# Kernel tuning notes

Measured on AMD Instinct MI355X. Metric: run time of the kernel, lower is better.

## Reference

```python
import jax, jax.numpy as jnp
import numpy as np
import math

D = 1024
H = 16
EPS = 1e-5

def _layernorm(x, gamma, beta):
    mu = jnp.mean(x, axis=-1, keepdims=True)
    var = jnp.var(x, axis=-1, keepdims=True)
    return (x - mu) * jax.lax.rsqrt(var + EPS) * gamma + beta

def setup_inputs() -> dict:
    key = jax.random.key(0)
    ks = jax.random.split(key, 6)
    B, T = 2, 2048
    x = jax.random.normal(ks[0], (B, T, D), dtype=jnp.float32)
    s = 1.0 / math.sqrt(D)
    Wq = jax.random.normal(ks[1], (D, D), dtype=jnp.float32) * s
    Wk = jax.random.normal(ks[2], (D, D), dtype=jnp.float32) * s
    Wv = jax.random.normal(ks[3], (D, D), dtype=jnp.float32) * s
    gamma = jnp.ones((D,), dtype=jnp.float32)
    beta = jnp.zeros((D,), dtype=jnp.float32)
    return {"x": x, "Wq": Wq, "Wk": Wk, "Wv": Wv, "gamma": gamma, "beta": beta}

def reference(x, Wq, Wk, Wv, gamma, beta):
    B, T, Dm = x.shape
    hd = Dm // H
    xn = _layernorm(x, gamma, beta)
    # torch Linear (no bias): y = x @ W.T
    q = (xn @ Wq.T).reshape(B, T, H, hd)
    k = (xn @ Wk.T).reshape(B, T, H, hd)
    v = (xn @ Wv.T).reshape(B, T, H, hd)
    scale = 1.0 / math.sqrt(hd)
    att = jnp.einsum('bnhd,bmhd->bnmh', q, k) * scale  # B,T,T,H
    w = jax.nn.softmax(att, axis=2)  # softmax over key dim m
    y = jnp.einsum('bnmh,bmhd->bnhd', w, v).reshape(B, T, Dm)
    return x + y
```

## Files before the change

kernel.cpp:

```cpp
#include <hip/hip_runtime.h>
#include <hip/hip_bf16.h>
#include <stdint.h>

#define D_MODEL 1024
#define T_SEQ   2048
#define NB      2
#define NH      16
#define HD      64
#define MTOK    4096

typedef __bf16  bf16x8 __attribute__((ext_vector_type(8)));
typedef float   f32x4  __attribute__((ext_vector_type(4)));
typedef float   f32x16 __attribute__((ext_vector_type(16)));

#define GPTR(p) ((const __attribute__((address_space(1))) void*)(p))
#define LPTR(p) ((__attribute__((address_space(3))) void*)(p))

static __device__ __forceinline__ ushort f2bf(float f) {
    union { float f; uint32_t u; } c{f};
    uint32_t u = c.u;
    return (ushort)((u + 0x7fff + ((u >> 16) & 1)) >> 16);
}

static __device__ __forceinline__ unsigned cvt_pk_bf16(float lo, float hi) {
    unsigned r;
    asm("v_cvt_pk_bf16_f32 %0, %1, %2" : "=v"(r) : "v"(lo), "v"(hi));
    return r;
}

#if defined(__has_builtin)
#if __has_builtin(__builtin_amdgcn_exp2f)
#define FEXP2(x) __builtin_amdgcn_exp2f(x)
#endif
#endif
#ifndef FEXP2
static __device__ __forceinline__ float fexp2_asm(float x) {
    float r;
    asm("v_exp_f32 %0, %1" : "=v"(r) : "v"(x));
    return r;
}
#define FEXP2(x) fexp2_asm(x)
#endif

__global__ __launch_bounds__(256) void ln_kernel(const float* __restrict__ x,
                                                 const float* __restrict__ gamma,
                                                 const float* __restrict__ beta,
                                                 ushort* __restrict__ xn) {
    int row = blockIdx.x;
    int tid = threadIdx.x;
    const float4* xr = (const float4*)(x + (size_t)row * D_MODEL);
    float4 v = xr[tid];
    float s  = v.x + v.y + v.z + v.w;
    float ss = v.x * v.x + v.y * v.y + v.z * v.z + v.w * v.w;
    #pragma unroll
    for (int m = 1; m < 64; m <<= 1) {
        s  += __shfl_xor(s, m);
        ss += __shfl_xor(ss, m);
    }
    __shared__ float red[8];
    int w = tid >> 6, lane = tid & 63;
    if (lane == 0) { red[w] = s; red[4 + w] = ss; }
    __syncthreads();
    s  = red[0] + red[1] + red[2] + red[3];
    ss = red[4] + red[5] + red[6] + red[7];
    float mu   = s * (1.0f / D_MODEL);
    float var  = ss * (1.0f / D_MODEL) - mu * mu;
    float rstd = rsqrtf(var + 1e-5f);
    float4 g = ((const float4*)gamma)[tid];
    float4 b = ((const float4*)beta)[tid];
    ushort4 o;
    o.x = f2bf((v.x - mu) * rstd * g.x + b.x);
    o.y = f2bf((v.y - mu) * rstd * g.y + b.y);
    o.z = f2bf((v.z - mu) * rstd * g.z + b.z);
    o.w = f2bf((v.w - mu) * rstd * g.w + b.w);
    ((ushort4*)(xn + (size_t)row * D_MODEL))[tid] = o;
}

__global__ __launch_bounds__(256) void cvt3_kernel(const float* __restrict__ a0,
                                                   const float* __restrict__ a1,
                                                   const float* __restrict__ a2,
                                                   ushort* __restrict__ o0,
                                                   ushort* __restrict__ o1,
                                                   ushort* __restrict__ o2) {
    int z = blockIdx.y;
    const float* a = (z == 0) ? a0 : (z == 1) ? a1 : a2;
    ushort* o = (z == 0) ? o0 : (z == 1) ? o1 : o2;
    int i = blockIdx.x * 256 + threadIdx.x;
    float4 v = ((const float4*)a)[i];
    ushort4 r;
    r.x = f2bf(v.x); r.y = f2bf(v.y); r.z = f2bf(v.z); r.w = f2bf(v.w);
    ((ushort4*)o)[i] = r;
}

__global__ __launch_bounds__(256) void gemm_qkv(const ushort* __restrict__ A,
                                                const ushort* __restrict__ w0,
                                                const ushort* __restrict__ w1,
                                                const ushort* __restrict__ w2,
                                                ushort* __restrict__ c0,
                                                ushort* __restrict__ c1,
                                                ushort* __restrict__ c2,
                                                int M, int N, int K) {
    const ushort* Bw = (blockIdx.z == 0) ? w0 : (blockIdx.z == 1) ? w1 : w2;
    ushort* C = (blockIdx.z == 0) ? c0 : (blockIdx.z == 1) ? c1 : c2;

    __shared__ __align__(16) ushort lA[2][128 * 64];
    __shared__ __align__(16) ushort lB[2][128 * 64];
    int tid = threadIdx.x;
    int w = tid >> 6, lane = tid & 63;
    int wr = w >> 1, wc = w & 1;
    int l15 = lane & 15, l4 = lane >> 4;
    int row0 = blockIdx.x * 128, col0 = blockIdx.y * 128;

    f32x4 zero = {0.f, 0.f, 0.f, 0.f};
    f32x4 acc[4][4];
    #pragma unroll
    for (int i = 0; i < 4; ++i)
        #pragma unroll
        for (int j = 0; j < 4; ++j) acc[i][j] = zero;

    int sr  = tid >> 3;
    int scc = (((tid & 7) ^ (sr & 7)) << 3);
    int rch[2];
    rch[0] = ((l4)     ^ (l15 & 7)) << 4;
    rch[1] = ((4 + l4) ^ (l15 & 7)) << 4;

    auto STAGE = [&](int buf, int kt) {
        int k0 = kt * 64;
        #pragma unroll
        for (int i = 0; i < 4; ++i) {
            int r = i * 32 + sr;
            const ushort* ga = A + (size_t)(row0 + r) * K + k0 + scc;
            __builtin_amdgcn_global_load_lds(GPTR(ga), LPTR((char*)lA[buf] + i * 4096 + tid * 16), 16, 0, 0);
            const ushort* gb = Bw + (size_t)(col0 + r) * K + k0 + scc;
            __builtin_amdgcn_global_load_lds(GPTR(gb), LPTR((char*)lB[buf] + i * 4096 + tid * 16), 16, 0, 0);
        }
    };

    STAGE(0, 0);
    __syncthreads();

    int buf = 0;
    const int NK = K / 64;
    for (int kt = 0; kt < NK; ++kt) {
        if (kt + 1 < NK) STAGE(buf ^ 1, kt + 1);
        const char* la  = (const char*)lA[buf];
        const char* lb_ = (const char*)lB[buf];
        __builtin_amdgcn_s_setprio(1);
        #pragma unroll
        for (int ks = 0; ks < 2; ++ks) {
            bf16x8 af[4], bfr[4];
            #pragma unroll
            for (int i = 0; i < 4; ++i) {
                int ra = wr * 64 + i * 16 + l15;
                int rb = wc * 64 + i * 16 + l15;
                af[i]  = *(const bf16x8*)(la  + ra * 128 + rch[ks]);
                bfr[i] = *(const bf16x8*)(lb_ + rb * 128 + rch[ks]);
            }
            #pragma unroll
            for (int i = 0; i < 4; ++i)
                #pragma unroll
                for (int j = 0; j < 4; ++j)
                    acc[i][j] = __builtin_amdgcn_mfma_f32_16x16x32_bf16(af[i], bfr[j], acc[i][j], 0, 0, 0);
        }
        __builtin_amdgcn_s_setprio(0);
        __syncthreads();
        buf ^= 1;
    }

    if (blockIdx.z == 2) {
        #pragma unroll
        for (int i = 0; i < 4; ++i) {
            int rbase = row0 + wr * 64 + i * 16 + l4 * 4;
            #pragma unroll
            for (int j = 0; j < 4; ++j) {
                int col = col0 + wc * 64 + j * 16 + l15;
                ushort4 o4;
                o4.x = f2bf(acc[i][j][0]);
                o4.y = f2bf(acc[i][j][1]);
                o4.z = f2bf(acc[i][j][2]);
                o4.w = f2bf(acc[i][j][3]);
                *(ushort4*)&C[(size_t)col * M + rbase] = o4;
            }
        }
    } else {
        float sc = (blockIdx.z == 0) ? 0.18033688011112042f : 1.0f;
        #pragma unroll
        for (int i = 0; i < 4; ++i) {
            int rbase = row0 + wr * 64 + i * 16 + l4 * 4;
            #pragma unroll
            for (int j = 0; j < 4; ++j) {
                int col = col0 + wc * 64 + j * 16 + l15;
                #pragma unroll
                for (int r = 0; r < 4; ++r)
                    C[(size_t)(rbase + r) * N + col] = f2bf(acc[i][j][r] * sc);
            }
        }
    }
}

__global__ __launch_bounds__(256, 2) void attn_kernel(const ushort* __restrict__ Q,
                                                      const ushort* __restrict__ Km,
                                                      const ushort* __restrict__ Vt,
                                                      const float* __restrict__ x,
                                                      float* __restrict__ out) {
    int bid = blockIdx.x;
    int sw  = (bid & 7) * 64 + (bid >> 3);
    int qt = sw & 15, h = (sw >> 4) & 15, b = sw >> 8;

    int tid = threadIdx.x, w = tid >> 6, lane = tid & 63;
    int l31 = lane & 31, hh = lane >> 5, x7 = lane & 7;
    size_t head_off = (size_t)b * T_SEQ * D_MODEL + (size_t)h * HD;
    const ushort* Qh  = Q  + head_off;
    const ushort* Kh  = Km + head_off;
    const ushort* Vth = Vt + (size_t)h * HD * MTOK + (size_t)b * T_SEQ;

    __shared__ __align__(16) ushort lK[4][64 * 64];
    __shared__ __align__(16) ushort lV[4][64 * 64];

    int qrow = qt * 128 + w * 32 + l31;
    bf16x8 qf[4];
    #pragma unroll
    for (int c = 0; c < 4; ++c)
        qf[c] = *(const bf16x8*)&Qh[(size_t)qrow * D_MODEL + hh * 8 + c * 16];

    int i0  = w * 128 + lane;
    int r0  = i0 >> 3;
    int cg0 = (i0 & 7) ^ (r0 & 7);
    const ushort* ksrc0 = Kh  + (size_t)r0 * D_MODEL + cg0 * 8;
    const ushort* ksrc1 = ksrc0 + (size_t)8 * D_MODEL;
    const ushort* vsrc0 = Vth + (size_t)r0 * MTOK + cg0 * 8;
    const ushort* vsrc1 = vsrc0 + (size_t)8 * MTOK;

    int chv[4];
    #pragma unroll
    for (int c = 0; c < 4; ++c) chv[c] = ((hh + 2 * c) ^ x7) << 4;

    f32x16 oa[2], ob[2], zvec;
    float la = 0.f, lb = 0.f;
    #pragma unroll
    for (int i = 0; i < 16; ++i) {
        oa[0][i] = 0.f; oa[1][i] = 0.f; ob[0][i] = 0.f; ob[1][i] = 0.f;
        zvec[i] = 0.f;
    }

    auto STAGE = [&](int t) {
        size_t kb = (size_t)t * 64;
        char* dk = (char*)lK[t & 3] + w * 2048;
        char* dv = (char*)lV[t & 3] + w * 2048;
        __builtin_amdgcn_global_load_lds(GPTR(ksrc0 + kb * D_MODEL), LPTR(dk), 16, 0, 0);
        __builtin_amdgcn_global_load_lds(GPTR(ksrc1 + kb * D_MODEL), LPTR(dk + 1024), 16, 0, 0);
        __builtin_amdgcn_global_load_lds(GPTR(vsrc0 + kb), LPTR(dv), 16, 0, 0);
        __builtin_amdgcn_global_load_lds(GPTR(vsrc1 + kb), LPTR(dv + 1024), 16, 0, 0);
    };

    auto QK = [&](int t, f32x16& sa, f32x16& sb) {
        const char* lKc = (const char*)lK[t & 3];
        __builtin_amdgcn_s_setprio(1);
        {
            bf16x8 ka  = *(const bf16x8*)(lKc + l31 * 128 + chv[0]);
            bf16x8 kb2 = *(const bf16x8*)(lKc + (32 + l31) * 128 + chv[0]);
            sa = __builtin_amdgcn_mfma_f32_32x32x16_bf16(ka,  qf[0], zvec, 0, 0, 0);
            sb = __builtin_amdgcn_mfma_f32_32x32x16_bf16(kb2, qf[0], zvec, 0, 0, 0);
        }
        #pragma unroll
        for (int c = 1; c < 4; ++c) {
            bf16x8 ka  = *(const bf16x8*)(lKc + l31 * 128 + chv[c]);
            bf16x8 kb2 = *(const bf16x8*)(lKc + (32 + l31) * 128 + chv[c]);
            sa = __builtin_amdgcn_mfma_f32_32x32x16_bf16(ka,  qf[c], sa, 0, 0, 0);
            sb = __builtin_amdgcn_mfma_f32_32x32x16_bf16(kb2, qf[c], sb, 0, 0, 0);
        }
        __builtin_amdgcn_s_setprio(0);
    };

    auto SMPV = [&](int t, const f32x16& sa, const f32x16& sb) {
        const char* lVc = (const char*)lV[t & 3];
        bf16x8 pfr[4];
        #pragma unroll
        for (int kbb = 0; kbb < 2; ++kbb) {
            float pr[16];
            #pragma unroll
            for (int r = 0; r < 16; ++r) pr[r] = FEXP2(kbb ? sb[r] : sa[r]);
            float s0 = (pr[0] + pr[1]) + (pr[2] + pr[3]);
            float s1 = (pr[4] + pr[5]) + (pr[6] + pr[7]);
            float s2 = (pr[8] + pr[9]) + (pr[10] + pr[11]);
            float s3 = (pr[12] + pr[13]) + (pr[14] + pr[15]);
            if (kbb == 0) la += (s0 + s1) + (s2 + s3);
            else          lb += (s0 + s1) + (s2 + s3);
            #pragma unroll
            for (int sl = 0; sl < 2; ++sl) {
                unsigned pA = cvt_pk_bf16(pr[sl * 8 + 0], pr[sl * 8 + 1]);
                unsigned pB = cvt_pk_bf16(pr[sl * 8 + 2], pr[sl * 8 + 3]);
                unsigned pC = cvt_pk_bf16(pr[sl * 8 + 4], pr[sl * 8 + 5]);
                unsigned pD = cvt_pk_bf16(pr[sl * 8 + 6], pr[sl * 8 + 7]);
                asm("v_permlane32_swap_b32 %0, %1" : "+v"(pA), "+v"(pC));
                asm("v_permlane32_swap_b32 %0, %1" : "+v"(pB), "+v"(pD));
                union { unsigned u[4]; bf16x8 v; } pf;
                pf.u[0] = pA; pf.u[1] = pB; pf.u[2] = pC; pf.u[3] = pD;
                pfr[kbb * 2 + sl] = pf.v;
            }
        }
        __builtin_amdgcn_s_setprio(1);
        #pragma unroll
        for (int ks = 0; ks < 4; ++ks) {
            #pragma unroll
            for (int dblk = 0; dblk < 2; ++dblk) {
                bf16x8 vf = *(const bf16x8*)(lVc + (dblk * 32 + l31) * 128 + chv[ks]);
                if (ks & 1)
                    ob[dblk] = __builtin_amdgcn_mfma_f32_32x32x16_bf16(vf, pfr[ks], ob[dblk], 0, 0, 0);
                else
                    oa[dblk] = __builtin_amdgcn_mfma_f32_32x32x16_bf16(vf, pfr[ks], oa[dblk], 0, 0, 0);
            }
        }
        __builtin_amdgcn_s_setprio(0);
    };

    STAGE(0);
    STAGE(1);
    __syncthreads();

    const int NT = T_SEQ / 64;
    for (int s = 0; s < NT / 2; ++s) {
        int t0 = 2 * s;
        if (s < NT / 2 - 1) { STAGE(t0 + 2); STAGE(t0 + 3); }
        f32x16 sa0, sb0, sa1, sb1;
        QK(t0, sa0, sb0);
        QK(t0 + 1, sa1, sb1);
        SMPV(t0, sa0, sb0);
        SMPV(t0 + 1, sa1, sb1);
        __syncthreads();
    }

    float Lt = la + lb;
    float Lfull = Lt + __shfl_xor(Lt, 32);
    float inv = 1.0f / Lfull;
    const float* xrow = x   + (size_t)(b * T_SEQ + qrow) * D_MODEL + h * HD + 4 * hh;
    float*       orow = out + (size_t)(b * T_SEQ + qrow) * D_MODEL + h * HD + 4 * hh;
    #pragma unroll
    for (int dblk = 0; dblk < 2; ++dblk) {
        #pragma unroll
        for (int g = 0; g < 4; ++g) {
            int coff = dblk * 32 + 8 * g;
            float4 xv = *(const float4*)(xrow + coff);
            float4 ov;
            ov.x = xv.x + (oa[dblk][4 * g + 0] + ob[dblk][4 * g + 0]) * inv;
            ov.y = xv.y + (oa[dblk][4 * g + 1] + ob[dblk][4 * g + 1]) * inv;
            ov.z = xv.z + (oa[dblk][4 * g + 2] + ob[dblk][4 * g + 2]) * inv;
            ov.w = xv.w + (oa[dblk][4 * g + 3] + ob[dblk][4 * g + 3]) * inv;
            *(float4*)(orow + coff) = ov;
        }
    }
}

extern "C" void kernel_launch(void* const* d_in, const int* in_sizes, int n_in,
                              void* d_out, int out_size, void* d_ws, size_t ws_size,
                              hipStream_t stream) {
    const float* x     = (const float*)d_in[0];
    const float* Wq    = (const float*)d_in[1];
    const float* Wk    = (const float*)d_in[2];
    const float* Wv    = (const float*)d_in[3];
    const float* gamma = (const float*)d_in[4];
    const float* beta  = (const float*)d_in[5];
    float* out = (float*)d_out;

    char* ws = (char*)d_ws;
    ushort* xn  = (ushort*)(ws);
    ushort* wqb = (ushort*)(ws + (8  << 20));
    ushort* wkb = (ushort*)(ws + (10 << 20));
    ushort* wvb = (ushort*)(ws + (12 << 20));
    ushort* Qb  = (ushort*)(ws + (14 << 20));
    ushort* Kb  = (ushort*)(ws + (22 << 20));
    ushort* Vtb = (ushort*)(ws + (30 << 20));

    int M = NB * T_SEQ;

    cvt3_kernel<<<dim3(1024, 3), 256, 0, stream>>>(Wq, Wk, Wv, wqb, wkb, wvb);
    ln_kernel<<<dim3(M), 256, 0, stream>>>(x, gamma, beta, xn);
    gemm_qkv<<<dim3(M / 128, D_MODEL / 128, 3), 256, 0, stream>>>(
        xn, wqb, wkb, wvb, Qb, Kb, Vtb, M, D_MODEL, D_MODEL);
    attn_kernel<<<dim3(512), 256, 0, stream>>>(Qb, Kb, Vtb, x, out);
}
```

Baseline: 99.86 us.

## Load K directly into registers and compute row sums via MFMA with ones

K tiles are no longer staged through LDS. Each wave now loads its K fragments straight from global memory into registers at the start of each iteration, which halves LDS traffic and LDS footprint. The per-row softmax denominator is now computed by an extra MFMA against an all-ones bf16 operand instead of scalar VALU adds and a cross-lane shuffle. The risks are exposed global-load latency for K, since the loads are issued right before use without prefetch, and a denominator summed from bf16-rounded probabilities rather than fp32 ones.

```diff
diff --git a/kernel.cpp b/kernel.cpp
--- a/kernel.cpp
+++ b/kernel.cpp
@@ -214,7 +214,6 @@
     const ushort* Kh  = Km + head_off;
     const ushort* Vth = Vt + (size_t)h * HD * MTOK + (size_t)b * T_SEQ;
 
-    __shared__ __align__(16) ushort lK[4][64 * 64];
     __shared__ __align__(16) ushort lV[4][64 * 64];
 
     int qrow = qt * 128 + w * 32 + l31;
@@ -222,12 +221,14 @@
     #pragma unroll
     for (int c = 0; c < 4; ++c)
         qf[c] = *(const bf16x8*)&Qh[(size_t)qrow * D_MODEL + hh * 8 + c * 16];
+
+    union { ushort u[8]; bf16x8 v; } onef;
+    #pragma unroll
+    for (int j = 0; j < 8; ++j) onef.u[j] = 0x3F80;
 
     int i0  = w * 128 + lane;
     int r0  = i0 >> 3;
     int cg0 = (i0 & 7) ^ (r0 & 7);
-    const ushort* ksrc0 = Kh  + (size_t)r0 * D_MODEL + cg0 * 8;
-    const ushort* ksrc1 = ksrc0 + (size_t)8 * D_MODEL;
     const ushort* vsrc0 = Vth + (size_t)r0 * MTOK + cg0 * 8;
     const ushort* vsrc1 = vsrc0 + (size_t)8 * MTOK;
 
@@ -235,39 +236,37 @@
     #pragma unroll
     for (int c = 0; c < 4; ++c) chv[c] = ((hh + 2 * c) ^ x7) << 4;
 
-    f32x16 oa[2], ob[2], zvec;
-    float la = 0.f, lb = 0.f;
+    f32x16 oa[2], ob[2], lacc, zvec;
     #pragma unroll
     for (int i = 0; i < 16; ++i) {
         oa[0][i] = 0.f; oa[1][i] = 0.f; ob[0][i] = 0.f; ob[1][i] = 0.f;
-        zvec[i] = 0.f;
+        lacc[i] = 0.f; zvec[i] = 0.f;
     }
 
     auto STAGE = [&](int t) {
         size_t kb = (size_t)t * 64;
-        char* dk = (char*)lK[t & 3] + w * 2048;
         char* dv = (char*)lV[t & 3] + w * 2048;
-        __builtin_amdgcn_global_load_lds(GPTR(ksrc0 + kb * D_MODEL), LPTR(dk), 16, 0, 0);
-        __builtin_amdgcn_global_load_lds(GPTR(ksrc1 + kb * D_MODEL), LPTR(dk + 1024), 16, 0, 0);
         __builtin_amdgcn_global_load_lds(GPTR(vsrc0 + kb), LPTR(dv), 16, 0, 0);
         __builtin_amdgcn_global_load_lds(GPTR(vsrc1 + kb), LPTR(dv + 1024), 16, 0, 0);
     };
 
-    auto QK = [&](int t, f32x16& sa, f32x16& sb) {
-        const char* lKc = (const char*)lK[t & 3];
+    auto KLOAD = [&](int t, bf16x8* kr) {
+        const ushort* Kt = Kh + (size_t)(t * 64) * D_MODEL;
+        #pragma unroll
+        for (int c = 0; c < 4; ++c) {
+            kr[c]     = *(const bf16x8*)&Kt[(size_t)l31 * D_MODEL + hh * 8 + c * 16];
+            kr[4 + c] = *(const bf16x8*)&Kt[(size_t)(32 + l31) * D_MODEL + hh * 8 + c * 16];
+        }
+    };
+
+    auto QKM = [&](const bf16x8* kr, f32x16& sa, f32x16& sb) {
         __builtin_amdgcn_s_setprio(1);
-        {
-            bf16x8 ka  = *(const bf16x8*)(lKc + l31 * 128 + chv[0]);
-            bf16x8 kb2 = *(const bf16x8*)(lKc + (32 + l31) * 128 + chv[0]);
-            sa = __builtin_amdgcn_mfma_f32_32x32x16_bf16(ka,  qf[0], zvec, 0, 0, 0);
-            sb = __builtin_amdgcn_mfma_f32_32x32x16_bf16(kb2, qf[0], zvec, 0, 0, 0);
-        }
+        sa = __builtin_amdgcn_mfma_f32_32x32x16_bf16(kr[0], qf[0], zvec, 0, 0, 0);
+        sb = __builtin_amdgcn_mfma_f32_32x32x16_bf16(kr[4], qf[0], zvec, 0, 0, 0);
         #pragma unroll
         for (int c = 1; c < 4; ++c) {
-            bf16x8 ka  = *(const bf16x8*)(lKc + l31 * 128 + chv[c]);
-            bf16x8 kb2 = *(const bf16x8*)(lKc + (32 + l31) * 128 + chv[c]);
-            sa = __builtin_amdgcn_mfma_f32_32x32x16_bf16(ka,  qf[c], sa, 0, 0, 0);
-            sb = __builtin_amdgcn_mfma_f32_32x32x16_bf16(kb2, qf[c], sb, 0, 0, 0);
+            sa = __builtin_amdgcn_mfma_f32_32x32x16_bf16(kr[c],     qf[c], sa, 0, 0, 0);
+            sb = __builtin_amdgcn_mfma_f32_32x32x16_bf16(kr[4 + c], qf[c], sb, 0, 0, 0);
         }
         __builtin_amdgcn_s_setprio(0);
     };
@@ -280,12 +279,6 @@
             float pr[16];
             #pragma unroll
             for (int r = 0; r < 16; ++r) pr[r] = FEXP2(kbb ? sb[r] : sa[r]);
-            float s0 = (pr[0] + pr[1]) + (pr[2] + pr[3]);
-            float s1 = (pr[4] + pr[5]) + (pr[6] + pr[7]);
-            float s2 = (pr[8] + pr[9]) + (pr[10] + pr[11]);
-            float s3 = (pr[12] + pr[13]) + (pr[14] + pr[15]);
-            if (kbb == 0) la += (s0 + s1) + (s2 + s3);
-            else          lb += (s0 + s1) + (s2 + s3);
             #pragma unroll
             for (int sl = 0; sl < 2; ++sl) {
                 unsigned pA = cvt_pk_bf16(pr[sl * 8 + 0], pr[sl * 8 + 1]);
@@ -310,6 +303,7 @@
                 else
                     oa[dblk] = __builtin_amdgcn_mfma_f32_32x32x16_bf16(vf, pfr[ks], oa[dblk], 0, 0, 0);
             }
+            lacc = __builtin_amdgcn_mfma_f32_32x32x16_bf16(onef.v, pfr[ks], lacc, 0, 0, 0);
         }
         __builtin_amdgcn_s_setprio(0);
     };
@@ -321,18 +315,19 @@
     const int NT = T_SEQ / 64;
     for (int s = 0; s < NT / 2; ++s) {
         int t0 = 2 * s;
+        bf16x8 kr0[8], kr1[8];
+        KLOAD(t0, kr0);
+        KLOAD(t0 + 1, kr1);
         if (s < NT / 2 - 1) { STAGE(t0 + 2); STAGE(t0 + 3); }
         f32x16 sa0, sb0, sa1, sb1;
-        QK(t0, sa0, sb0);
-        QK(t0 + 1, sa1, sb1);
+        QKM(kr0, sa0, sb0);
+        QKM(kr1, sa1, sb1);
         SMPV(t0, sa0, sb0);
         SMPV(t0 + 1, sa1, sb1);
         __syncthreads();
     }
 
-    float Lt = la + lb;
-    float Lfull = Lt + __shfl_xor(Lt, 32);
-    float inv = 1.0f / Lfull;
+    float inv = 1.0f / lacc[0];
     const float* xrow = x   + (size_t)(b * T_SEQ + qrow) * D_MODEL + h * HD + 4 * hh;
     float*       orow = out + (size_t)(b * T_SEQ + qrow) * D_MODEL + h * HD + 4 * hh;
     #pragma unroll
```

Result: slower. 137.8 us (+38.0%).
